# Performance work log

Hardware: AMD Instinct MI355X
Metric: run time of the kernel (lower is better)

Reference implementation:

```python
import jax, jax.numpy as jnp
import numpy as np

NUM_EXPERTS = 8
TOP_K = 2
TOKENS = 4096
HIDDEN = 1024
INTER = 2048
INIT_STD = 0.01  # nnx.initializers.normal() default stddev


def setup_inputs() -> dict:
    key = jax.random.key(0)
    k1, k2, k3, k4, k5 = jax.random.split(key, 5)
    return {
        "inputs": jax.random.normal(k1, (TOKENS, HIDDEN), jnp.float32),
        "router_logits": jax.random.normal(k2, (TOKENS, NUM_EXPERTS), jnp.float32),
        "wi_0": jax.random.normal(k3, (NUM_EXPERTS, HIDDEN, INTER), jnp.float32) * INIT_STD,
        "wi_1": jax.random.normal(k4, (NUM_EXPERTS, HIDDEN, INTER), jnp.float32) * INIT_STD,
        "wo": jax.random.normal(k5, (NUM_EXPERTS, INTER, HIDDEN), jnp.float32) * INIT_STD,
    }


def reference(inputs, router_logits, wi_0, wi_1, wo):
    T, H = inputs.shape
    # --- top-k routing ---
    top_k_logits, top_k_indices = jax.lax.top_k(router_logits, TOP_K)  # [T, k]
    w = jax.nn.softmax(top_k_logits, axis=-1)
    w = w / jnp.sum(w, axis=-1, keepdims=True)  # (redundant renorm, kept faithful)
    # --- permute: sort token-expert pairs by expert id ---
    flat_experts = top_k_indices.reshape(-1)          # [T*k]
    sort_idx = jnp.argsort(flat_experts)              # stable sort -> token order within group
    token_idx = sort_idx // TOP_K                     # source token of each sorted slot
    x = inputs[token_idx]                             # [T*k, H] gathered/permuted tokens
    group_sizes = jnp.bincount(flat_experts, length=NUM_EXPERTS).astype(jnp.int32)
    # --- grouped (ragged) GEMM experts: silu(x@wi_0) * (x@wi_1) @ wo ---
    h0 = jax.lax.ragged_dot(x, wi_0, group_sizes, preferred_element_type=jnp.float32)
    h1 = jax.lax.ragged_dot(x, wi_1, group_sizes, preferred_element_type=jnp.float32)
    act = jax.nn.silu(h0) * h1                        # [T*k, INTER]
    y = jax.lax.ragged_dot(act, wo, group_sizes, preferred_element_type=jnp.float32)  # [T*k, H]
    # --- unpermute + weighted combine over top-k ---
    unsort = jnp.argsort(sort_idx)
    y = y[unsort].reshape(T, TOP_K, H)
    return jnp.sum(y * w[..., None], axis=1)          # [T, H]
```

## Files before the change

kernel.cpp:

```cpp
#include <hip/hip_runtime.h>
#include <hip/hip_bf16.h>

#define T_TOKENS 4096
#define HID 1024
#define INTER 2048
#define NEXP 8
#define TOPK 2
#define RTOT (T_TOKENS * TOPK)
#define BMT 128
#define BN 128
#define MAXT (RTOT / BMT + NEXP)

typedef __attribute__((ext_vector_type(8))) short bf16x8;
typedef __attribute__((ext_vector_type(4))) float f32x4;

typedef __attribute__((address_space(1))) const unsigned int gu32;
typedef __attribute__((address_space(3))) unsigned int lu32;

__device__ __forceinline__ void gl16(const void* g, void* l) {
  __builtin_amdgcn_global_load_lds((gu32*)g, (lu32*)l, 16, 0, 0);
}

__device__ __forceinline__ unsigned f2bf(float f) {
  union { float f; unsigned u; } v; v.f = f;
  unsigned u = v.u;
  return (u + 0x7FFFu + ((u >> 16) & 1u)) >> 16;
}

__device__ __forceinline__ float bf2f(unsigned short s) {
  union { unsigned u; float f; } v; v.u = ((unsigned)s) << 16;
  return v.f;
}

__device__ __forceinline__ int swz(int row, int kb) {
  return row * 128 + (kb ^ ((row & 7) << 4));
}

__device__ __forceinline__ void phase_barrier() {
  asm volatile("" ::: "memory");
  __builtin_amdgcn_s_barrier();
  asm volatile("" ::: "memory");
}

__global__ __launch_bounds__(1024)
void k_routing(const float* __restrict__ logits, int* ntiles,
               int* te2, int* tr02, int* tcnt2,
               float* pw, int* rows, float* rw, int* slotOf) {
  __shared__ int cnt[NEXP];
  __shared__ int cur[NEXP];
  const int tid = threadIdx.x;
  if (tid < NEXP) cnt[tid] = 0;
  __syncthreads();

  int myE[4][2];
  float myW[4][2];
#pragma unroll
  for (int j = 0; j < 4; ++j) {
    int t = j * 1024 + tid;
    float l[NEXP];
#pragma unroll
    for (int i = 0; i < NEXP; ++i) l[i] = logits[t * NEXP + i];
    int i0 = 0; float b0 = l[0];
#pragma unroll
    for (int i = 1; i < NEXP; ++i) if (l[i] > b0) { b0 = l[i]; i0 = i; }
    int i1 = -1; float b1 = -1e30f;
#pragma unroll
    for (int i = 0; i < NEXP; ++i) if (i != i0 && l[i] > b1) { b1 = l[i]; i1 = i; }
    float e = __expf(b1 - b0);
    float w0 = 1.f / (1.f + e);
    float w1 = e / (1.f + e);
    myE[j][0] = i0; myE[j][1] = i1;
    myW[j][0] = w0; myW[j][1] = w1;
    pw[2 * t] = w0; pw[2 * t + 1] = w1;
#pragma unroll
    for (int ex = 0; ex < NEXP; ++ex) {
      int c = __popcll(__ballot(i0 == ex)) + __popcll(__ballot(i1 == ex));
      if ((tid & 63) == 0 && c) atomicAdd(&cnt[ex], c);
    }
  }
  __syncthreads();

  if (tid == 0) {
    int off = 0, nm = 0;
    for (int e = 0; e < NEXP; ++e) {
      int c = cnt[e];
      cur[e] = off;
      for (int m0 = 0; m0 < c; m0 += BMT) {
        te2[nm] = e; tr02[nm] = off + m0; tcnt2[nm] = min(BMT, c - m0); ++nm;
      }
      off += c;
    }
    ntiles[1] = nm;
  }
  __syncthreads();

#pragma unroll
  for (int j = 0; j < 4; ++j) {
    int t = j * 1024 + tid;
#pragma unroll
    for (int k = 0; k < TOPK; ++k) {
      int e = myE[j][k];
      int s = atomicAdd(&cur[e], 1);
      rows[s] = t;
      rw[s] = myW[j][k];
      slotOf[2 * t + k] = s;
    }
  }
}

__global__ __launch_bounds__(256)
void k_prep(const float* __restrict__ X, unsigned short* __restrict__ Xb,
            const float* __restrict__ W0, const float* __restrict__ W1,
            const float* __restrict__ WO,
            unsigned short* __restrict__ T0, unsigned short* __restrict__ T1,
            unsigned short* __restrict__ To) {
  int bid = blockIdx.x;
  const int tid = threadIdx.x;
  if (bid < 1024) {
    int base = bid * 1024 + tid;
#pragma unroll
    for (int j = 0; j < 4; ++j) {
      int i = base + j * 256;
      float4 v = *(const float4*)(X + (size_t)i * 4);
      uint2 p;
      p.x = f2bf(v.x) | (f2bf(v.y) << 16);
      p.y = f2bf(v.z) | (f2bf(v.w) << 16);
      *(uint2*)(Xb + (size_t)i * 4) = p;
    }
    return;
  }
  bid -= 1024;
  const int w = bid >> 11;
  const int r = bid & 2047;
  const float* W = (w == 0) ? W0 : (w == 1) ? W1 : WO;
  unsigned short* T = (w == 0) ? T0 : (w == 1) ? T1 : To;
  int K, N, KT2, NT, kt, nt, e;
  if (w < 2) { K = HID;   N = INTER; KT2 = 16; NT = 16; kt = r & 15; nt = (r >> 4) & 15; e = r >> 8; }
  else       { K = INTER; N = HID;   KT2 = 32; NT = 8;  kt = r & 31; nt = (r >> 5) & 7;  e = r >> 8; }
  __shared__ float ls[64 * 128];
  const float* src = W + (size_t)e * K * N + (size_t)(kt * 64) * N + nt * 128;
#pragma unroll
  for (int t = 0; t < 8; ++t) {
    int u = t * 256 + tid;
    int k = u >> 5, n4 = u & 31;
    float4 v = *(const float4*)(src + (size_t)k * N + n4 * 4);
    *(float4*)(ls + k * 128 + ((n4 ^ ((k >> 3) & 7)) << 2)) = v;
  }
  __syncthreads();
  unsigned short* dst = T + (((size_t)e * NT + nt) * KT2 + kt) * 8192;
#pragma unroll
  for (int t = 0; t < 4; ++t) {
    int v = t * 256 + tid;
    int kt2 = v >> 9, n = (v >> 2) & 127, sw = v & 3;
    int kc = kt2 * 4 + (sw ^ ((n >> 1) & 3));
    const float* col = ls + (size_t)(kc * 8) * 128 +
                       (((n >> 2) ^ (kc & 7)) << 2) + (n & 3);
    unsigned b[8];
#pragma unroll
    for (int i = 0; i < 8; ++i) b[i] = f2bf(col[i * 128]);
    uint4 q;
    q.x = b[0] | (b[1] << 16); q.y = b[2] | (b[3] << 16);
    q.z = b[4] | (b[5] << 16); q.w = b[6] | (b[7] << 16);
    *(uint4*)(dst + (size_t)v * 8) = q;
  }
}

__global__ __launch_bounds__(512, 4)
void k_gemm1n(const unsigned short* __restrict__ Xb,
              const unsigned short* __restrict__ WT0,
              const unsigned short* __restrict__ WT1,
              const int* __restrict__ ntiles, const int* __restrict__ te2,
              const int* __restrict__ tr02, const int* __restrict__ tcnt2,
              const int* __restrict__ rows,
              unsigned short* __restrict__ act) {
  const int ty = blockIdx.y;
  if (ty >= ntiles[1]) return;
  const int e = te2[ty], row0 = tr02[ty], mcnt = tcnt2[ty];
  const int nt = blockIdx.x, n0 = nt * BN;
  const int tid = threadIdx.x, lane = tid & 63, wv = tid >> 6;
  const int mh = wv >> 2, nq = wv & 3;
  const int l15 = lane & 15, sl = lane >> 4;

  __shared__ unsigned char sm[49152];

  const int am = tid >> 2;
  const int atok = rows[row0 + (am < mcnt ? am : mcnt - 1)];
  const int askc = ((tid & 3) ^ ((tid >> 3) & 3)) * 8;
  const unsigned short* B0t = WT0 + ((size_t)e * 16 + nt) * 32 * 4096;
  const unsigned short* B1t = WT1 + ((size_t)e * 16 + nt) * 32 * 4096;

  int aoff[4], boff[2];
#pragma unroll
  for (int f = 0; f < 4; ++f) {
    int m = mh * 64 + f * 16 + l15;
    aoff[f] = m * 64 + ((sl ^ ((m >> 1) & 3)) << 4);
  }
#pragma unroll
  for (int g = 0; g < 2; ++g) {
    int n = nq * 32 + g * 16 + l15;
    boff[g] = n * 64 + ((sl ^ ((n >> 1) & 3)) << 4);
  }

  f32x4 acc0[4][2], acc1[4][2];
  const f32x4 zz = {0.f, 0.f, 0.f, 0.f};
#pragma unroll
  for (int f = 0; f < 4; ++f)
#pragma unroll
    for (int g = 0; g < 2; ++g) { acc0[f][g] = zz; acc1[f][g] = zz; }

  const int NT_K = HID / 32;

  gl16(Xb + (size_t)atok * HID + askc, sm + tid * 16);
  gl16(B0t + (size_t)tid * 8, sm + 8192 + tid * 16);
  gl16(B1t + (size_t)tid * 8, sm + 16384 + tid * 16);

  for (int t = 0; t < NT_K; ++t) {
    unsigned char* cur = sm + (t & 1) * 24576;
    unsigned char* nxt = sm + ((t + 1) & 1) * 24576;
    const int tn = (t + 1 < NT_K) ? (t + 1) : (NT_K - 1);

    gl16(Xb + (size_t)atok * HID + tn * 32 + askc, nxt + tid * 16);
    gl16(B0t + (size_t)tn * 4096 + tid * 8, nxt + 8192 + tid * 16);
    gl16(B1t + (size_t)tn * 4096 + tid * 8, nxt + 16384 + tid * 16);
    asm volatile("s_waitcnt vmcnt(3)" ::: "memory");
    __builtin_amdgcn_sched_barrier(0);
    phase_barrier();

    bf16x8 aA[4], b0q[2], b1q[2];
#pragma unroll
    for (int g = 0; g < 2; ++g) {
      b0q[g] = *(const bf16x8*)(cur + 8192 + boff[g]);
      b1q[g] = *(const bf16x8*)(cur + 16384 + boff[g]);
    }
#pragma unroll
    for (int f = 0; f < 4; ++f) aA[f] = *(const bf16x8*)(cur + aoff[f]);
    __builtin_amdgcn_s_setprio(1);
#pragma unroll
    for (int f = 0; f < 4; ++f)
#pragma unroll
      for (int g = 0; g < 2; ++g) {
        acc0[f][g] = __builtin_amdgcn_mfma_f32_16x16x32_bf16(aA[f], b0q[g], acc0[f][g], 0, 0, 0);
        acc1[f][g] = __builtin_amdgcn_mfma_f32_16x16x32_bf16(aA[f], b1q[g], acc1[f][g], 0, 0, 0);
      }
    __builtin_amdgcn_s_setprio(0);
    phase_barrier();
  }

#pragma unroll
  for (int f = 0; f < 4; ++f) {
#pragma unroll
    for (int r = 0; r < 4; ++r) {
      int m = mh * 64 + f * 16 + sl * 4 + r;
      if (m >= mcnt) continue;
      size_t base = (size_t)(row0 + m) * INTER + n0 + nq * 32 + l15;
#pragma unroll
      for (int g = 0; g < 2; ++g) {
        float h0 = acc0[f][g][r];
        float h1 = acc1[f][g][r];
        float s = h0 / (1.f + __expf(-h0));
        act[base + g * 16] = (unsigned short)f2bf(s * h1);
      }
    }
  }
}

__global__ __launch_bounds__(256, 4)
void k_gemm2n(const unsigned short* __restrict__ act,
              const unsigned short* __restrict__ WTo,
              const int* __restrict__ ntiles, const int* __restrict__ te2,
              const int* __restrict__ tr02, const int* __restrict__ tcnt2,
              unsigned short* __restrict__ y) {
  const int ty = blockIdx.y;
  if (ty >= ntiles[1]) return;
  const int e = te2[ty], row0 = tr02[ty], mcnt = tcnt2[ty];
  const int nt = blockIdx.x, n0 = nt * BN;
  const int tid = threadIdx.x, lane = tid & 63, wv = tid >> 6;
  const int wr = wv >> 1, wc = wv & 1;
  const int l15 = lane & 15, sl = lane >> 4;

  __shared__ unsigned char sm[32768];

  const int am0 = tid >> 2, am1 = 64 + (tid >> 2);
  const int ar0 = row0 + (am0 < mcnt ? am0 : mcnt - 1);
  const int ar1 = row0 + (am1 < mcnt ? am1 : mcnt - 1);
  const int askc = ((tid & 3) ^ ((tid >> 3) & 3)) * 8;
  const unsigned short* Bt = WTo + ((size_t)e * 8 + nt) * 64 * 4096;

  int aoff[4], boff[4];
#pragma unroll
  for (int f = 0; f < 4; ++f) {
    int m = wr * 64 + f * 16 + l15;
    aoff[f] = m * 64 + ((sl ^ ((m >> 1) & 3)) << 4);
    int n = wc * 64 + f * 16 + l15;
    boff[f] = n * 64 + ((sl ^ ((n >> 1) & 3)) << 4);
  }

  f32x4 acc[4][4];
  const f32x4 zz = {0.f, 0.f, 0.f, 0.f};
#pragma unroll
  for (int i = 0; i < 4; ++i)
#pragma unroll
    for (int j = 0; j < 4; ++j) acc[i][j] = zz;

  const int NT_K = INTER / 32;

  gl16(act + (size_t)ar0 * INTER + askc, sm + tid * 16);
  gl16(act + (size_t)ar1 * INTER + askc, sm + (256 + tid) * 16);
  gl16(Bt + (size_t)tid * 8, sm + 8192 + tid * 16);
  gl16(Bt + (size_t)(256 + tid) * 8, sm + 8192 + (256 + tid) * 16);

  for (int t = 0; t < NT_K; ++t) {
    unsigned char* cur = sm + (t & 1) * 16384;
    unsigned char* nxt = sm + ((t + 1) & 1) * 16384;
    const int tn = (t + 1 < NT_K) ? (t + 1) : (NT_K - 1);

    gl16(act + (size_t)ar0 * INTER + tn * 32 + askc, nxt + tid * 16);
    gl16(act + (size_t)ar1 * INTER + tn * 32 + askc, nxt + (256 + tid) * 16);
    gl16(Bt + (size_t)tn * 4096 + tid * 8, nxt + 8192 + tid * 16);
    gl16(Bt + ((size_t)tn * 4096 + 2048) + tid * 8, nxt + 8192 + (256 + tid) * 16);
    asm volatile("s_waitcnt vmcnt(4)" ::: "memory");
    __builtin_amdgcn_sched_barrier(0);
    phase_barrier();

    bf16x8 af[4], bb[4];
#pragma unroll
    for (int f = 0; f < 4; ++f) {
      af[f] = *(const bf16x8*)(cur + aoff[f]);
      bb[f] = *(const bf16x8*)(cur + 8192 + boff[f]);
    }
    __builtin_amdgcn_s_setprio(1);
#pragma unroll
    for (int mf = 0; mf < 4; ++mf)
#pragma unroll
      for (int nf = 0; nf < 4; ++nf)
        acc[mf][nf] = __builtin_amdgcn_mfma_f32_16x16x32_bf16(af[mf], bb[nf], acc[mf][nf], 0, 0, 0);
    __builtin_amdgcn_s_setprio(0);
    phase_barrier();
  }

#pragma unroll
  for (int mf = 0; mf < 4; ++mf) {
#pragma unroll
    for (int r = 0; r < 4; ++r) {
      int m = wr * 64 + mf * 16 + sl * 4 + r;
      if (m >= mcnt) continue;
      unsigned short* yp = y + (size_t)(row0 + m) * HID + n0 + wc * 64 + l15;
#pragma unroll
      for (int nf = 0; nf < 4; ++nf)
        yp[nf * 16] = (unsigned short)f2bf(acc[mf][nf][r]);
    }
  }
}

__global__ void k_combine(const unsigned short* __restrict__ y,
                          const float* __restrict__ pw,
                          const int* __restrict__ slotOf,
                          float* __restrict__ out) {
  int idx = blockIdx.x * blockDim.x + threadIdx.x;
  int t = idx >> 7, hc = (idx & 127) * 8;
  int s0 = slotOf[2 * t], s1 = slotOf[2 * t + 1];
  float w0 = pw[2 * t], w1 = pw[2 * t + 1];
  uint4 a = *(const uint4*)(y + (size_t)s0 * HID + hc);
  uint4 b = *(const uint4*)(y + (size_t)s1 * HID + hc);
  float o[8];
  const unsigned* ap = (const unsigned*)&a;
  const unsigned* bp = (const unsigned*)&b;
#pragma unroll
  for (int i = 0; i < 4; ++i) {
    o[2 * i]     = w0 * bf2f((unsigned short)(ap[i] & 0xFFFF)) + w1 * bf2f((unsigned short)(bp[i] & 0xFFFF));
    o[2 * i + 1] = w0 * bf2f((unsigned short)(ap[i] >> 16))    + w1 * bf2f((unsigned short)(bp[i] >> 16));
  }
  float* op = out + (size_t)t * HID + hc;
  *(float4*)op = make_float4(o[0], o[1], o[2], o[3]);
  *(float4*)(op + 4) = make_float4(o[4], o[5], o[6], o[7]);
}

__global__ __launch_bounds__(256, 2)
void k_gemm1_fb(const float* __restrict__ X, const float* __restrict__ W0,
                const float* __restrict__ W1, const int* __restrict__ ntiles,
                const int* __restrict__ te2, const int* __restrict__ tr02,
                const int* __restrict__ tcnt2, const int* __restrict__ rows,
                unsigned short* __restrict__ act) {
  const int ty = blockIdx.y;
  if (ty >= ntiles[1]) return;
  const int e = te2[ty], row0 = tr02[ty], mcnt = tcnt2[ty];
  const int n0 = blockIdx.x * BN;
  const int tid = threadIdx.x;
  const int lane = tid & 63, wv = tid >> 6;
  const int wr = wv >> 1, wc = wv & 1;

  __shared__ unsigned char smf[49152];
  unsigned char* As = smf;
  unsigned char* B0s = smf + 16384;
  unsigned char* B1s = smf + 32768;

  int atok[8];
#pragma unroll
  for (int j = 0; j < 8; ++j) {
    int m = (j * 256 + tid) >> 4;
    atok[j] = (m < mcnt) ? rows[row0 + m] : -1;
  }
  const int bnb = (tid & 7) | ((tid >> 7) << 6);
  const int bc = (tid >> 3) & 15;

  f32x4 acc0[4][4], acc1[4][4];
  const f32x4 zz = {0.f, 0.f, 0.f, 0.f};
#pragma unroll
  for (int i = 0; i < 4; ++i)
#pragma unroll
    for (int j = 0; j < 4; ++j) { acc0[i][j] = zz; acc1[i][j] = zz; }

  const float* W0e = W0 + (size_t)e * HID * INTER + n0;
  const float* W1e = W1 + (size_t)e * HID * INTER + n0;

  for (int k0 = 0; k0 < HID; k0 += 64) {
#pragma unroll
    for (int j = 0; j < 8; ++j) {
      int c = j * 256 + tid;
      int m = c >> 4, ch = c & 15;
      float4 v = make_float4(0.f, 0.f, 0.f, 0.f);
      int tok = atok[j];
      if (tok >= 0) v = *(const float4*)(X + (size_t)tok * HID + k0 + 4 * ch);
      uint2 p;
      p.x = f2bf(v.x) | (f2bf(v.y) << 16);
      p.y = f2bf(v.z) | (f2bf(v.w) << 16);
      *(uint2*)(As + swz(m, 8 * ch)) = p;
    }
#pragma unroll
    for (int j = 0; j < 8; ++j) {
      int n = bnb | (j << 3);
      const float* p0 = W0e + (size_t)(k0 + 4 * bc) * INTER + n;
      float a0 = p0[0], a1 = p0[INTER], a2 = p0[2 * INTER], a3 = p0[3 * INTER];
      uint2 q;
      q.x = f2bf(a0) | (f2bf(a1) << 16);
      q.y = f2bf(a2) | (f2bf(a3) << 16);
      *(uint2*)(B0s + swz(n, 8 * bc)) = q;
      const float* p1 = W1e + (size_t)(k0 + 4 * bc) * INTER + n;
      a0 = p1[0]; a1 = p1[INTER]; a2 = p1[2 * INTER]; a3 = p1[3 * INTER];
      q.x = f2bf(a0) | (f2bf(a1) << 16);
      q.y = f2bf(a2) | (f2bf(a3) << 16);
      *(uint2*)(B1s + swz(n, 8 * bc)) = q;
    }
    __syncthreads();
#pragma unroll
    for (int kq = 0; kq < 2; ++kq) {
      int kb = kq * 64 + 16 * (lane >> 4);
      bf16x8 a[4], b0[4], b1[4];
#pragma unroll
      for (int f = 0; f < 4; ++f) {
        int m = wr * 64 + f * 16 + (lane & 15);
        a[f] = *(const bf16x8*)(As + swz(m, kb));
        int n = wc * 64 + f * 16 + (lane & 15);
        b0[f] = *(const bf16x8*)(B0s + swz(n, kb));
        b1[f] = *(const bf16x8*)(B1s + swz(n, kb));
      }
#pragma unroll
      for (int mf = 0; mf < 4; ++mf)
#pragma unroll
        for (int nf = 0; nf < 4; ++nf) {
          acc0[mf][nf] = __builtin_amdgcn_mfma_f32_16x16x32_bf16(a[mf], b0[nf], acc0[mf][nf], 0, 0, 0);
          acc1[mf][nf] = __builtin_amdgcn_mfma_f32_16x16x32_bf16(a[mf], b1[nf], acc1[mf][nf], 0, 0, 0);
        }
    }
    __syncthreads();
  }
#pragma unroll
  for (int mf = 0; mf < 4; ++mf) {
#pragma unroll
    for (int r = 0; r < 4; ++r) {
      int m = wr * 64 + mf * 16 + (lane >> 4) * 4 + r;
      if (m >= mcnt) continue;
      size_t rowbase = (size_t)(row0 + m) * INTER + n0 + wc * 64 + (lane & 15);
#pragma unroll
      for (int nf = 0; nf < 4; ++nf) {
        float h0 = acc0[mf][nf][r];
        float h1 = acc1[mf][nf][r];
        float s = h0 / (1.f + __expf(-h0));
        act[rowbase + nf * 16] = (unsigned short)f2bf(s * h1);
      }
    }
  }
}

__global__ __launch_bounds__(256, 2)
void k_gemm2_fb(const unsigned short* __restrict__ act, const float* __restrict__ WO,
                const int* __restrict__ ntiles, const int* __restrict__ te2,
                const int* __restrict__ tr02, const int* __restrict__ tcnt2,
                const int* __restrict__ rows, const float* __restrict__ rw,
                float* __restrict__ out) {
  const int ty = blockIdx.y;
  if (ty >= ntiles[1]) return;
  const int e = te2[ty], row0 = tr02[ty], mcnt = tcnt2[ty];
  const int n0 = blockIdx.x * BN;
  const int tid = threadIdx.x;
  const int lane = tid & 63, wv = tid >> 6;
  const int wr = wv >> 1, wc = wv & 1;

  __shared__ unsigned char smf[32768];
  unsigned char* As = smf;
  unsigned char* Bs = smf + 16384;

  const int bnb = (tid & 7) | ((tid >> 7) << 6);
  const int bc = (tid >> 3) & 15;

  f32x4 acc[4][4];
  const f32x4 zz = {0.f, 0.f, 0.f, 0.f};
#pragma unroll
  for (int i = 0; i < 4; ++i)
#pragma unroll
    for (int j = 0; j < 4; ++j) acc[i][j] = zz;

  const float* We = WO + (size_t)e * INTER * HID + n0;

  for (int k0 = 0; k0 < INTER; k0 += 64) {
#pragma unroll
    for (int j = 0; j < 4; ++j) {
      int u = j * 256 + tid;
      int m = u >> 3, ch = u & 7;
      uint4 v = make_uint4(0u, 0u, 0u, 0u);
      if (m < mcnt)
        v = *(const uint4*)(act + (size_t)(row0 + m) * INTER + k0 + 8 * ch);
      *(uint4*)(As + swz(m, 16 * ch)) = v;
    }
#pragma unroll
    for (int j = 0; j < 8; ++j) {
      int n = bnb | (j << 3);
      const float* p = We + (size_t)(k0 + 4 * bc) * HID + n;
      float a0 = p[0], a1 = p[HID], a2 = p[2 * HID], a3 = p[3 * HID];
      uint2 q;
      q.x = f2bf(a0) | (f2bf(a1) << 16);
      q.y = f2bf(a2) | (f2bf(a3) << 16);
      *(uint2*)(Bs + swz(n, 8 * bc)) = q;
    }
    __syncthreads();
#pragma unroll
    for (int kq = 0; kq < 2; ++kq) {
      int kb = kq * 64 + 16 * (lane >> 4);
      bf16x8 a[4], b[4];
#pragma unroll
      for (int f = 0; f < 4; ++f) {
        int m = wr * 64 + f * 16 + (lane & 15);
        a[f] = *(const bf16x8*)(As + swz(m, kb));
        int n = wc * 64 + f * 16 + (lane & 15);
        b[f] = *(const bf16x8*)(Bs + swz(n, kb));
      }
#pragma unroll
      for (int mf = 0; mf < 4; ++mf)
#pragma unroll
        for (int nf = 0; nf < 4; ++nf)
          acc[mf][nf] = __builtin_amdgcn_mfma_f32_16x16x32_bf16(a[mf], b[nf], acc[mf][nf], 0, 0, 0);
    }
    __syncthreads();
  }
#pragma unroll
  for (int mf = 0; mf < 4; ++mf) {
#pragma unroll
    for (int r = 0; r < 4; ++r) {
      int m = wr * 64 + mf * 16 + (lane >> 4) * 4 + r;
      if (m >= mcnt) continue;
      int tok = rows[row0 + m];
      float w = rw[row0 + m];
      float* op = out + (size_t)tok * HID + n0 + wc * 64 + (lane & 15);
#pragma unroll
      for (int nf = 0; nf < 4; ++nf)
        atomicAdd(op + nf * 16, w * acc[mf][nf][r]);
    }
  }
}

extern "C" void kernel_launch(void* const* d_in, const int* in_sizes, int n_in,
                              void* d_out, int out_size, void* d_ws, size_t ws_size,
                              hipStream_t stream) {
  const float* X  = (const float*)d_in[0];
  const float* RL = (const float*)d_in[1];
  const float* W0 = (const float*)d_in[2];
  const float* W1 = (const float*)d_in[3];
  const float* WOp = (const float*)d_in[4];
  float* out = (float*)d_out;

  char* ws = (char*)d_ws;
  int* ntiles  = (int*)(ws + 128);
  int* te2     = (int*)(ws + 2048);
  int* tr02    = (int*)(ws + 2560);
  int* tcnt2   = (int*)(ws + 3072);
  float* pw    = (float*)(ws + 8192 + 32768);
  int* rows    = (int*)(ws + 8192 + 65536);
  float* rw    = (float*)(ws + 8192 + 98304);
  int* slotOf  = (int*)(ws + 8192 + 131072);

  const bool big = ws_size >= ((size_t)145 << 20);

  k_routing<<<1, 1024, 0, stream>>>(RL, ntiles, te2, tr02, tcnt2, pw, rows, rw, slotOf);

  if (big) {
    unsigned short* Xb  = (unsigned short*)(ws + ((size_t)1 << 20));
    unsigned short* act = (unsigned short*)(ws + ((size_t)16 << 20));
    unsigned short* WT0 = (unsigned short*)(ws + ((size_t)48 << 20));
    unsigned short* WT1 = (unsigned short*)(ws + ((size_t)80 << 20));
    unsigned short* WTo = (unsigned short*)(ws + ((size_t)112 << 20));
    unsigned short* y   = (unsigned short*)(ws + ((size_t)48 << 20));

    k_prep<<<7168, 256, 0, stream>>>(X, Xb, W0, W1, WOp, WT0, WT1, WTo);

    k_gemm1n<<<dim3(INTER / BN, MAXT), 512, 0, stream>>>(Xb, WT0, WT1, ntiles, te2, tr02, tcnt2, rows, act);
    k_gemm2n<<<dim3(HID / BN, MAXT), 256, 0, stream>>>(act, WTo, ntiles, te2, tr02, tcnt2, y);
    k_combine<<<(T_TOKENS * HID / 8) / 256, 256, 0, stream>>>(y, pw, slotOf, out);
  } else {
    unsigned short* act = (unsigned short*)(ws + ((size_t)1 << 20));
    hipMemsetAsync(d_out, 0, (size_t)out_size * sizeof(float), stream);
    k_gemm1_fb<<<dim3(INTER / BN, MAXT), 256, 0, stream>>>(X, W0, W1, ntiles, te2, tr02, tcnt2, rows, act);
    k_gemm2_fb<<<dim3(HID / BN, MAXT), 256, 0, stream>>>(act, WOp, ntiles, te2, tr02, tcnt2, rows, rw, out);
  }
}
```

Before: 220.7 us.

## Overlap WO weight conversion with first grouped GEMM by folding into its grid

Splits the weight-prep kernel so that only X, W0 and W1 are converted before the first GEMM. The WO transpose and bf16 conversion becomes 128 extra block rows of the first GEMM launch, so that memory-bound work can share the GPU with the compute-bound GEMM tiles. It also changes the LDS swizzle in the staging buffer (psig), likely to reduce bank conflicts. The risk is that the conversion blocks compete with GEMM blocks for occupancy and bandwidth, and they are scheduled after the GEMM rows by block index.

```diff
diff --git a/kernel.cpp b/kernel.cpp
--- a/kernel.cpp
+++ b/kernel.cpp
@@ -42,6 +42,8 @@
   asm volatile("" ::: "memory");
 }
 
+__device__ __forceinline__ int psig(int kap) { return kap ^ ((kap & 1) << 2); }
+
 __global__ __launch_bounds__(1024)
 void k_routing(const float* __restrict__ logits, int* ntiles,
                int* te2, int* tr02, int* tcnt2,
@@ -109,11 +111,9 @@
 }
 
 __global__ __launch_bounds__(256)
-void k_prep(const float* __restrict__ X, unsigned short* __restrict__ Xb,
-            const float* __restrict__ W0, const float* __restrict__ W1,
-            const float* __restrict__ WO,
-            unsigned short* __restrict__ T0, unsigned short* __restrict__ T1,
-            unsigned short* __restrict__ To) {
+void k_prep1(const float* __restrict__ X, unsigned short* __restrict__ Xb,
+             const float* __restrict__ W0, const float* __restrict__ W1,
+             unsigned short* __restrict__ T0, unsigned short* __restrict__ T1) {
   int bid = blockIdx.x;
   const int tid = threadIdx.x;
   if (bid < 1024) {
@@ -132,29 +132,27 @@
   bid -= 1024;
   const int w = bid >> 11;
   const int r = bid & 2047;
-  const float* W = (w == 0) ? W0 : (w == 1) ? W1 : WO;
-  unsigned short* T = (w == 0) ? T0 : (w == 1) ? T1 : To;
-  int K, N, KT2, NT, kt, nt, e;
-  if (w < 2) { K = HID;   N = INTER; KT2 = 16; NT = 16; kt = r & 15; nt = (r >> 4) & 15; e = r >> 8; }
-  else       { K = INTER; N = HID;   KT2 = 32; NT = 8;  kt = r & 31; nt = (r >> 5) & 7;  e = r >> 8; }
+  const float* W = (w == 0) ? W0 : W1;
+  unsigned short* T = (w == 0) ? T0 : T1;
+  const int kt = r & 15, nt = (r >> 4) & 15, e = r >> 8;
   __shared__ float ls[64 * 128];
-  const float* src = W + (size_t)e * K * N + (size_t)(kt * 64) * N + nt * 128;
+  const float* src = W + (size_t)e * HID * INTER + (size_t)(kt * 64) * INTER + nt * 128;
 #pragma unroll
   for (int t = 0; t < 8; ++t) {
     int u = t * 256 + tid;
     int k = u >> 5, n4 = u & 31;
-    float4 v = *(const float4*)(src + (size_t)k * N + n4 * 4);
-    *(float4*)(ls + k * 128 + ((n4 ^ ((k >> 3) & 7)) << 2)) = v;
+    float4 v = *(const float4*)(src + (size_t)k * INTER + n4 * 4);
+    *(float4*)(ls + k * 128 + ((n4 ^ psig(k >> 3)) << 2)) = v;
   }
   __syncthreads();
-  unsigned short* dst = T + (((size_t)e * NT + nt) * KT2 + kt) * 8192;
+  unsigned short* dst = T + (((size_t)e * 16 + nt) * 16 + kt) * 8192;
 #pragma unroll
   for (int t = 0; t < 4; ++t) {
     int v = t * 256 + tid;
     int kt2 = v >> 9, n = (v >> 2) & 127, sw = v & 3;
     int kc = kt2 * 4 + (sw ^ ((n >> 1) & 3));
     const float* col = ls + (size_t)(kc * 8) * 128 +
-                       (((n >> 2) ^ (kc & 7)) << 2) + (n & 3);
+                       (((n >> 2) ^ psig(kc)) << 2) + (n & 3);
     unsigned b[8];
 #pragma unroll
     for (int i = 0; i < 8; ++i) b[i] = f2bf(col[i * 128]);
@@ -166,22 +164,58 @@
 }
 
 __global__ __launch_bounds__(512, 4)
-void k_gemm1n(const unsigned short* __restrict__ Xb,
+void k_gemm1w(const unsigned short* __restrict__ Xb,
               const unsigned short* __restrict__ WT0,
               const unsigned short* __restrict__ WT1,
+              const float* __restrict__ WO,
+              unsigned short* __restrict__ WTo,
               const int* __restrict__ ntiles, const int* __restrict__ te2,
               const int* __restrict__ tr02, const int* __restrict__ tcnt2,
               const int* __restrict__ rows,
               unsigned short* __restrict__ act) {
   const int ty = blockIdx.y;
+  const int nt = blockIdx.x;
+  const int tid = threadIdx.x;
+  __shared__ __align__(16) unsigned char sm[49152];
+
+  if (ty >= MAXT) {
+    const int r = (ty - MAXT) * 16 + nt;
+    const int kt = r & 31, ntt = (r >> 5) & 7, e = r >> 8;
+    float* ls = (float*)sm;
+    const float* src = WO + (size_t)e * INTER * HID + (size_t)(kt * 64) * HID + ntt * 128;
+#pragma unroll
+    for (int t = 0; t < 4; ++t) {
+      int u = t * 512 + tid;
+      int k = u >> 5, n4 = u & 31;
+      float4 v = *(const float4*)(src + (size_t)k * HID + n4 * 4);
+      *(float4*)(ls + k * 128 + ((n4 ^ psig(k >> 3)) << 2)) = v;
+    }
+    __syncthreads();
+    unsigned short* dst = WTo + (((size_t)e * 8 + ntt) * 32 + kt) * 8192;
+#pragma unroll
+    for (int t = 0; t < 2; ++t) {
+      int v = t * 512 + tid;
+      int kt2 = v >> 9, n = (v >> 2) & 127, sw = v & 3;
+      int kc = kt2 * 4 + (sw ^ ((n >> 1) & 3));
+      const float* col = ls + (size_t)(kc * 8) * 128 +
+                         (((n >> 2) ^ psig(kc)) << 2) + (n & 3);
+      unsigned b[8];
+#pragma unroll
+      for (int i = 0; i < 8; ++i) b[i] = f2bf(col[i * 128]);
+      uint4 q;
+      q.x = b[0] | (b[1] << 16); q.y = b[2] | (b[3] << 16);
+      q.z = b[4] | (b[5] << 16); q.w = b[6] | (b[7] << 16);
+      *(uint4*)(dst + (size_t)v * 8) = q;
+    }
+    return;
+  }
+
   if (ty >= ntiles[1]) return;
   const int e = te2[ty], row0 = tr02[ty], mcnt = tcnt2[ty];
-  const int nt = blockIdx.x, n0 = nt * BN;
-  const int tid = threadIdx.x, lane = tid & 63, wv = tid >> 6;
+  const int n0 = nt * BN;
+  const int lane = tid & 63, wv = tid >> 6;
   const int mh = wv >> 2, nq = wv & 3;
   const int l15 = lane & 15, sl = lane >> 4;
-
-  __shared__ unsigned char sm[49152];
 
   const int am = tid >> 2;
   const int atok = rows[row0 + (am < mcnt ? am : mcnt - 1)];
@@ -278,7 +312,7 @@
   const int wr = wv >> 1, wc = wv & 1;
   const int l15 = lane & 15, sl = lane >> 4;
 
-  __shared__ unsigned char sm[32768];
+  __shared__ __align__(16) unsigned char sm[32768];
 
   const int am0 = tid >> 2, am1 = 64 + (tid >> 2);
   const int ar0 = row0 + (am0 < mcnt ? am0 : mcnt - 1);
@@ -600,9 +634,10 @@
     unsigned short* WTo = (unsigned short*)(ws + ((size_t)112 << 20));
     unsigned short* y   = (unsigned short*)(ws + ((size_t)48 << 20));
 
-    k_prep<<<7168, 256, 0, stream>>>(X, Xb, W0, W1, WOp, WT0, WT1, WTo);
-
-    k_gemm1n<<<dim3(INTER / BN, MAXT), 512, 0, stream>>>(Xb, WT0, WT1, ntiles, te2, tr02, tcnt2, rows, act);
+    k_prep1<<<5120, 256, 0, stream>>>(X, Xb, W0, W1, WT0, WT1);
+
+    k_gemm1w<<<dim3(INTER / BN, MAXT + 128), 512, 0, stream>>>(
+        Xb, WT0, WT1, WOp, WTo, ntiles, te2, tr02, tcnt2, rows, act);
     k_gemm2n<<<dim3(HID / BN, MAXT), 256, 0, stream>>>(act, WTo, ntiles, te2, tr02, tcnt2, y);
     k_combine<<<(T_TOKENS * HID / 8) / 256, 256, 0, stream>>>(y, pw, slotOf, out);
   } else {
```

Result: faster. 215.4 us (-2.4%).
